# Performance work log

Measured on AMD Instinct MI355X. Metric: run time of the kernel, lower is better.

Reference implementation:

```python
import jax, jax.numpy as jnp
import numpy as np

SCALE = 0.02
EPS = 1e-5


def setup_inputs() -> dict:
    key = jax.random.key(0)
    ks = jax.random.split(key, 11)
    C = 256
    inp = {
        "x": jax.random.normal(ks[0], (64, C, 28, 28), dtype=jnp.float32),
        "w1": jax.random.normal(ks[1], (C, C, 3, 3), dtype=jnp.float32) * 0.05,
        "g1": jax.random.uniform(ks[2], (C,), dtype=jnp.float32, minval=0.5, maxval=1.5),
        "b1": jax.random.normal(ks[3], (C,), dtype=jnp.float32) * 0.1,
        "m1": jax.random.normal(ks[4], (C,), dtype=jnp.float32) * 0.1,
        "v1": jax.random.uniform(ks[5], (C,), dtype=jnp.float32, minval=0.5, maxval=1.5),
        "w2": jax.random.normal(ks[6], (C, C, 3, 3), dtype=jnp.float32) * 0.05,
        "g2": jax.random.uniform(ks[7], (C,), dtype=jnp.float32, minval=0.5, maxval=1.5),
        "b2": jax.random.normal(ks[8], (C,), dtype=jnp.float32) * 0.1,
        "m2": jax.random.normal(ks[9], (C,), dtype=jnp.float32) * 0.1,
        "v2": jax.random.uniform(ks[10], (C,), dtype=jnp.float32, minval=0.5, maxval=1.5),
    }
    return inp


def _bin_conv3x3(x, w, stride=1):
    # 1-bit weight conv: sign(w)*scale, straight-through estimator for grads.
    wb = w + jax.lax.stop_gradient(jnp.sign(w) - w)
    y = jax.lax.conv_general_dilated(
        x, wb,
        window_strides=(stride, stride),
        padding=[(1, 1), (1, 1)],
        dimension_numbers=("NCHW", "OIHW", "NCHW"),
    )
    return y * SCALE


def _bn(x, g, b, m, v):
    # eval-mode batchnorm with running stats
    inv = g * jax.lax.rsqrt(v + EPS)  # [C]
    return x * inv[None, :, None, None] + (b - m * inv)[None, :, None, None]


def reference(x, w1, g1, b1, m1, v1, w2, g2, b2, m2, v2):
    out = jax.nn.relu(_bn(_bin_conv3x3(x, w1, 1), g1, b1, m1, v1))
    out = _bn(_bin_conv3x3(out, w2, 1), g2, b2, m2, v2)
    return jax.nn.relu(out + x)
```

## Files before the change

### kernel.cpp

```cpp
#include <hip/hip_runtime.h>

#define EPS_F 1e-5f
#define SCALE_F 0.02f

using short8  = __attribute__((ext_vector_type(8))) short;
using floatx4 = __attribute__((ext_vector_type(4))) float;

__device__ __forceinline__ unsigned short f2bf(float f) {
  unsigned u = __float_as_uint(f);
  return (unsigned short)((u + 0x7fffu + ((u >> 16) & 1u)) >> 16);
}

__global__ void prep_w(const float* __restrict__ w1, const float* __restrict__ w2,
                       unsigned short* __restrict__ ap1, unsigned short* __restrict__ ap2,
                       const float* g1, const float* b1, const float* m1, const float* v1,
                       const float* g2, const float* b2, const float* m2, const float* v2,
                       float* bnp) {
  const float* __restrict__ w = blockIdx.y ? w2 : w1;
  unsigned short* __restrict__ ap = blockIdx.y ? ap2 : ap1;
  int t = blockIdx.x * 256 + threadIdx.x;
  int off = t >> 13;
  int c8  = (t >> 8) & 31;
  int co  = t & 255;
  const float* ws = w + (size_t)(co * 256 + c8 * 8) * 9 + off;
  short8 o;
#pragma unroll
  for (int j = 0; j < 8; ++j) {
    float v = ws[j * 9];
    o[j] = (v > 0.f) ? (short)0x3F80 : ((v < 0.f) ? (short)0xBF80 : (short)0);
  }
  *(short8*)(ap + (size_t)t * 8) = o;
  if (blockIdx.x == 0 && blockIdx.y == 0) {
    int c = threadIdx.x;
    float i1 = g1[c] * rsqrtf(v1[c] + EPS_F);
    bnp[c]       = SCALE_F * i1;
    bnp[256 + c] = b1[c] - m1[c] * i1;
    float i2 = g2[c] * rsqrtf(v2[c] + EPS_F);
    bnp[512 + c] = SCALE_F * i2;
    bnp[768 + c] = b2[c] - m2[c] * i2;
  }
}

__global__ void prep_x(const float* __restrict__ x, unsigned short* __restrict__ xb,
                       unsigned short* __restrict__ abuf) {
  int h = blockIdx.x;
  int n = blockIdx.y;
  int tid = threadIdx.x;
  const float* xs = x + ((size_t)n * 256 + tid) * 784 + h * 28;
  unsigned short* xd = xb + ((size_t)n * 900 + (h + 1) * 30 + 1) * 256 + tid;
#pragma unroll
  for (int p4 = 0; p4 < 7; ++p4) {
    floatx4 f = *(const floatx4*)(xs + p4 * 4);
#pragma unroll
    for (int k = 0; k < 4; ++k)
      xd[(size_t)(p4 * 4 + k) * 256] = f2bf(f[k]);
  }
  {
    int bufi = tid >> 7, side = (tid >> 6) & 1, c4 = tid & 63;
    unsigned short* bb = (bufi ? abuf : xb) + ((size_t)n * 900 + (h + 1) * 30 + side * 29) * 256;
    ushort4 z = {0, 0, 0, 0};
    *(ushort4*)(bb + c4 * 4) = z;
  }
  if (h == 0 || h == 27) {
    int row = (h == 0) ? 0 : 29;
    for (int u = tid; u < 3840; u += 256) {
      int bufi = u / 1920;
      int r    = u - bufi * 1920;
      int px   = r >> 6, c4 = r & 63;
      unsigned short* bb = (bufi ? abuf : xb) + ((size_t)n * 900 + row * 30 + px) * 256;
      ushort4 z = {0, 0, 0, 0};
      *(ushort4*)(bb + c4 * 4) = z;
    }
  }
}

template<int STAGE>
__global__ __launch_bounds__(256, 2) void bconv(
    const unsigned short* __restrict__ Bin,
    const unsigned short* __restrict__ Apack,
    const float* __restrict__ bnp,
    unsigned short* __restrict__ aout,
    const float* __restrict__ xres,
    float* __restrict__ out)
{
  __shared__ __align__(16) unsigned short smem[STAGE == 1 ? 29568 : 11520];
  unsigned short* Blds = smem;

  const int tid  = threadIdx.x;
  const int lane = tid & 63;
  const int wv   = tid >> 6;
  const int quad = lane >> 4;
  const int l16  = lane & 15;
  const int spBlk = blockIdx.x;
  const int n     = blockIdx.y;

  const int prow0 = 4 * spBlk;
  const unsigned short* bsrc = Bin + ((size_t)n * 900 + prow0 * 30) * 256;
  const int coW = wv * 64;

  int pxS[7];
#pragma unroll
  for (int s = 0; s < 7; ++s) {
    int lm = s * 16 + l16;
    int hl = lm / 28;
    int w  = lm - hl * 28;
    pxS[s] = hl * 30 + w;
  }

  floatx4 acc[4][7];
#pragma unroll
  for (int c = 0; c < 4; ++c)
#pragma unroll
    for (int s = 0; s < 7; ++s)
      acc[c][s] = (floatx4){0.f, 0.f, 0.f, 0.f};

#pragma unroll 1
  for (int cb = 0; cb < 4; ++cb) {
    __syncthreads();
    for (int u = tid; u < 1440; u += 256) {
      int px = u >> 3, c = u & 7;
      const unsigned short* src = bsrc + (size_t)px * 256 + cb * 64 + c * 8;
      *(short8*)&Blds[(px << 6) + ((c ^ (px & 7)) << 3)] = *(const short8*)src;
    }
    __syncthreads();

    const int cq = cb * 8 + quad;
#pragma unroll 1
    for (int kh = 0; kh < 3; ++kh) {
#pragma unroll
      for (int kw = 0; kw < 3; ++kw) {
        const int D = kh * 30 + kw;
        const int chunk0 = (kh * 3 + kw) * 32 + cq;
#pragma unroll
        for (int half = 0; half < 2; ++half) {
          const int chunk = chunk0 + half * 4;
          const unsigned short* apb = Apack + ((size_t)(chunk * 256 + coW + l16)) * 8;
          short8 a0 = *(const short8*)(apb);
          short8 a1 = *(const short8*)(apb + 16 * 8);
          short8 a2 = *(const short8*)(apb + 32 * 8);
          short8 a3 = *(const short8*)(apb + 48 * 8);
          const int C = half * 4 + quad;
#pragma unroll
          for (int s = 0; s < 7; ++s) {
            int pe = pxS[s] + D;
            short8 b = *(const short8*)&Blds[(pe << 6) + ((C ^ (pe & 7)) << 3)];
            acc[0][s] = __builtin_amdgcn_mfma_f32_16x16x32_bf16(a0, b, acc[0][s], 0, 0, 0);
            acc[1][s] = __builtin_amdgcn_mfma_f32_16x16x32_bf16(a1, b, acc[1][s], 0, 0, 0);
            acc[2][s] = __builtin_amdgcn_mfma_f32_16x16x32_bf16(a2, b, acc[2][s], 0, 0, 0);
            acc[3][s] = __builtin_amdgcn_mfma_f32_16x16x32_bf16(a3, b, acc[3][s], 0, 0, 0);
          }
        }
      }
    }
  }

  if (STAGE == 1) {
    __syncthreads();
#pragma unroll
    for (int c = 0; c < 4; ++c) {
      int co = coW + c * 16 + quad * 4;
      floatx4 As = *(const floatx4*)(bnp + co);
      floatx4 Bs = *(const floatx4*)(bnp + 256 + co);
#pragma unroll
      for (int s = 0; s < 7; ++s) {
        int px = s * 16 + l16;
        ushort4 o;
        o.x = f2bf(fmaxf(acc[c][s][0] * As[0] + Bs[0], 0.f));
        o.y = f2bf(fmaxf(acc[c][s][1] * As[1] + Bs[1], 0.f));
        o.z = f2bf(fmaxf(acc[c][s][2] * As[2] + Bs[2], 0.f));
        o.w = f2bf(fmaxf(acc[c][s][3] * As[3] + Bs[3], 0.f));
        *(ushort4*)&smem[px * 264 + co] = o;
      }
    }
    __syncthreads();
    unsigned short* dst0 = aout + ((size_t)n * 900 + (prow0 + 1) * 30 + 1) * 256;
    for (int u = tid; u < 3584; u += 256) {
      int px = u >> 5;
      int c8 = (u & 31) * 8;
      int r  = px / 28;
      int w  = px - r * 28;
      *(short8*)(dst0 + (size_t)(r * 30 + w) * 256 + c8) = *(const short8*)&smem[px * 264 + c8];
    }
  } else {
#pragma unroll
    for (int c = 0; c < 4; ++c) {
      int co = coW + c * 16 + quad * 4;
      floatx4 As = *(const floatx4*)(bnp + 512 + co);
      floatx4 Bs = *(const floatx4*)(bnp + 768 + co);
#pragma unroll
      for (int s = 0; s < 7; ++s) {
        int m = spBlk * 112 + s * 16 + l16;
#pragma unroll
        for (int r = 0; r < 4; ++r) {
          size_t oidx = ((size_t)n * 256 + co + r) * 784 + m;
          float v = acc[c][s][r] * As[r] + Bs[r] + xres[oidx];
          out[oidx] = fmaxf(v, 0.f);
        }
      }
    }
  }
}


extern "C" void kernel_launch(void* const* d_in, const int* in_sizes, int n_in,
                              void* d_out, int out_size, void* d_ws, size_t ws_size,
                              hipStream_t stream) {
  const float* x  = (const float*)d_in[0];
  const float* w1 = (const float*)d_in[1];
  const float* g1 = (const float*)d_in[2];
  const float* b1 = (const float*)d_in[3];
  const float* m1 = (const float*)d_in[4];
  const float* v1 = (const float*)d_in[5];
  const float* w2 = (const float*)d_in[6];
  const float* g2 = (const float*)d_in[7];
  const float* b2 = (const float*)d_in[8];
  const float* m2 = (const float*)d_in[9];
  const float* v2 = (const float*)d_in[10];
  float* out = (float*)d_out;

  char* ws = (char*)d_ws;
  const size_t PADBUF = (size_t)64 * 900 * 256 * 2;
  const size_t WPACK  = 589824ull * 2;
  unsigned short* xb   = (unsigned short*)ws;
  unsigned short* abuf = (unsigned short*)(ws + PADBUF);
  unsigned short* ap1  = (unsigned short*)(ws + 2 * PADBUF);
  unsigned short* ap2  = (unsigned short*)(ws + 2 * PADBUF + WPACK);
  float* bnp           = (float*)(ws + 2 * PADBUF + 2 * WPACK);

  prep_w<<<dim3(288, 2), 256, 0, stream>>>(w1, w2, ap1, ap2,
                                           g1, b1, m1, v1, g2, b2, m2, v2, bnp);
  prep_x<<<dim3(28, 64), 256, 0, stream>>>(x, xb, abuf);

  dim3 grid(7, 64);
  bconv<1><<<grid, 256, 0, stream>>>(xb,   ap1, bnp, abuf, nullptr, nullptr);
  bconv<2><<<grid, 256, 0, stream>>>(abuf, ap2, bnp, nullptr, x, out);
}
```

Before: 252.1 us.

## Retile conv blocks to two images by 128 channels and merge prep kernels

Each conv block now covers two images (224 pixels) and 128 output channels instead of one image and all 256 channels, and the grid gains a z dimension for the channel half. Each wave holds 2x14 accumulators instead of 4x7, so it loads half as many weight fragments per MFMA group and reuses each LDS B fragment across fewer MFMAs. The two prep kernels are fused into one launch to remove a launch. The trade-off is that more LDS B reads happen per MFMA, the activation tile is loaded twice (once per channel half), and stage 1 uses one smem size for both stages, which may affect occupancy.

```diff
diff --git a/kernel.cpp b/kernel.cpp
--- a/kernel.cpp
+++ b/kernel.cpp
@@ -11,41 +11,44 @@
   return (unsigned short)((u + 0x7fffu + ((u >> 16) & 1u)) >> 16);
 }
 
-__global__ void prep_w(const float* __restrict__ w1, const float* __restrict__ w2,
-                       unsigned short* __restrict__ ap1, unsigned short* __restrict__ ap2,
-                       const float* g1, const float* b1, const float* m1, const float* v1,
-                       const float* g2, const float* b2, const float* m2, const float* v2,
-                       float* bnp) {
-  const float* __restrict__ w = blockIdx.y ? w2 : w1;
-  unsigned short* __restrict__ ap = blockIdx.y ? ap2 : ap1;
-  int t = blockIdx.x * 256 + threadIdx.x;
-  int off = t >> 13;
-  int c8  = (t >> 8) & 31;
-  int co  = t & 255;
-  const float* ws = w + (size_t)(co * 256 + c8 * 8) * 9 + off;
-  short8 o;
-#pragma unroll
-  for (int j = 0; j < 8; ++j) {
-    float v = ws[j * 9];
-    o[j] = (v > 0.f) ? (short)0x3F80 : ((v < 0.f) ? (short)0xBF80 : (short)0);
-  }
-  *(short8*)(ap + (size_t)t * 8) = o;
-  if (blockIdx.x == 0 && blockIdx.y == 0) {
-    int c = threadIdx.x;
-    float i1 = g1[c] * rsqrtf(v1[c] + EPS_F);
-    bnp[c]       = SCALE_F * i1;
-    bnp[256 + c] = b1[c] - m1[c] * i1;
-    float i2 = g2[c] * rsqrtf(v2[c] + EPS_F);
-    bnp[512 + c] = SCALE_F * i2;
-    bnp[768 + c] = b2[c] - m2[c] * i2;
-  }
-}
-
-__global__ void prep_x(const float* __restrict__ x, unsigned short* __restrict__ xb,
-                       unsigned short* __restrict__ abuf) {
-  int h = blockIdx.x;
-  int n = blockIdx.y;
+__global__ void prep_all(const float* __restrict__ x,
+                         unsigned short* __restrict__ xb, unsigned short* __restrict__ abuf,
+                         const float* __restrict__ w1, const float* __restrict__ w2,
+                         unsigned short* __restrict__ ap1, unsigned short* __restrict__ ap2,
+                         const float* g1, const float* b1, const float* m1, const float* v1,
+                         const float* g2, const float* b2, const float* m2, const float* v2,
+                         float* bnp) {
+  int bid = blockIdx.x;
   int tid = threadIdx.x;
+  if (bid < 576) {
+    const float* __restrict__ w = (bid >= 288) ? w2 : w1;
+    unsigned short* __restrict__ ap = (bid >= 288) ? ap2 : ap1;
+    int t = (bid >= 288 ? bid - 288 : bid) * 256 + tid;
+    int off = t >> 13;
+    int c8  = (t >> 8) & 31;
+    int co  = t & 255;
+    const float* wsrc = w + (size_t)(co * 256 + c8 * 8) * 9 + off;
+    short8 o;
+#pragma unroll
+    for (int j = 0; j < 8; ++j) {
+      float v = wsrc[j * 9];
+      o[j] = (v > 0.f) ? (short)0x3F80 : ((v < 0.f) ? (short)0xBF80 : (short)0);
+    }
+    *(short8*)(ap + (size_t)t * 8) = o;
+    if (bid == 0) {
+      int c = tid;
+      float i1 = g1[c] * rsqrtf(v1[c] + EPS_F);
+      bnp[c]       = SCALE_F * i1;
+      bnp[256 + c] = b1[c] - m1[c] * i1;
+      float i2 = g2[c] * rsqrtf(v2[c] + EPS_F);
+      bnp[512 + c] = SCALE_F * i2;
+      bnp[768 + c] = b2[c] - m2[c] * i2;
+    }
+    return;
+  }
+  int bid2 = bid - 576;
+  int n = bid2 / 28;
+  int h = bid2 - n * 28;
   const float* xs = x + ((size_t)n * 256 + tid) * 784 + h * 28;
   unsigned short* xd = xb + ((size_t)n * 900 + (h + 1) * 30 + 1) * 256 + tid;
 #pragma unroll
@@ -83,7 +86,7 @@
     const float* __restrict__ xres,
     float* __restrict__ out)
 {
-  __shared__ __align__(16) unsigned short smem[STAGE == 1 ? 29568 : 11520];
+  __shared__ __align__(16) unsigned short smem[23040];
   unsigned short* Blds = smem;
 
   const int tid  = threadIdx.x;
@@ -92,34 +95,39 @@
   const int quad = lane >> 4;
   const int l16  = lane & 15;
   const int spBlk = blockIdx.x;
-  const int n     = blockIdx.y;
+  const int n0    = blockIdx.y * 2;
+  const int coB   = blockIdx.z;
+  const int coBase = coB * 128;
 
   const int prow0 = 4 * spBlk;
-  const unsigned short* bsrc = Bin + ((size_t)n * 900 + prow0 * 30) * 256;
-  const int coW = wv * 64;
-
-  int pxS[7];
-#pragma unroll
-  for (int s = 0; s < 7; ++s) {
-    int lm = s * 16 + l16;
-    int hl = lm / 28;
-    int w  = lm - hl * 28;
-    pxS[s] = hl * 30 + w;
-  }
-
-  floatx4 acc[4][7];
-#pragma unroll
-  for (int c = 0; c < 4; ++c)
-#pragma unroll
-    for (int s = 0; s < 7; ++s)
+  const unsigned short* bsrc = Bin + ((size_t)n0 * 900 + prow0 * 30) * 256;
+  const int coW = coBase + wv * 32;
+
+  int pxS[14];
+#pragma unroll
+  for (int s = 0; s < 14; ++s) {
+    int lm  = s * 16 + l16;
+    int img = lm >= 112;
+    int lmL = lm - 112 * img;
+    int hl  = lmL / 28;
+    int w   = lmL - hl * 28;
+    pxS[s] = img * 180 + hl * 30 + w;
+  }
+
+  floatx4 acc[2][14];
+#pragma unroll
+  for (int c = 0; c < 2; ++c)
+#pragma unroll
+    for (int s = 0; s < 14; ++s)
       acc[c][s] = (floatx4){0.f, 0.f, 0.f, 0.f};
 
 #pragma unroll 1
   for (int cb = 0; cb < 4; ++cb) {
     __syncthreads();
-    for (int u = tid; u < 1440; u += 256) {
+    for (int u = tid; u < 2880; u += 256) {
       int px = u >> 3, c = u & 7;
-      const unsigned short* src = bsrc + (size_t)px * 256 + cb * 64 + c * 8;
+      int imgo = (px >= 180) ? (230400 - 180 * 256) : 0;
+      const unsigned short* src = bsrc + imgo + (size_t)px * 256 + cb * 64 + c * 8;
       *(short8*)&Blds[(px << 6) + ((c ^ (px & 7)) << 3)] = *(const short8*)src;
     }
     __syncthreads();
@@ -137,17 +145,13 @@
           const unsigned short* apb = Apack + ((size_t)(chunk * 256 + coW + l16)) * 8;
           short8 a0 = *(const short8*)(apb);
           short8 a1 = *(const short8*)(apb + 16 * 8);
-          short8 a2 = *(const short8*)(apb + 32 * 8);
-          short8 a3 = *(const short8*)(apb + 48 * 8);
           const int C = half * 4 + quad;
 #pragma unroll
-          for (int s = 0; s < 7; ++s) {
+          for (int s = 0; s < 14; ++s) {
             int pe = pxS[s] + D;
             short8 b = *(const short8*)&Blds[(pe << 6) + ((C ^ (pe & 7)) << 3)];
             acc[0][s] = __builtin_amdgcn_mfma_f32_16x16x32_bf16(a0, b, acc[0][s], 0, 0, 0);
             acc[1][s] = __builtin_amdgcn_mfma_f32_16x16x32_bf16(a1, b, acc[1][s], 0, 0, 0);
-            acc[2][s] = __builtin_amdgcn_mfma_f32_16x16x32_bf16(a2, b, acc[2][s], 0, 0, 0);
-            acc[3][s] = __builtin_amdgcn_mfma_f32_16x16x32_bf16(a3, b, acc[3][s], 0, 0, 0);
           }
         }
       }
@@ -157,42 +161,51 @@
   if (STAGE == 1) {
     __syncthreads();
 #pragma unroll
-    for (int c = 0; c < 4; ++c) {
-      int co = coW + c * 16 + quad * 4;
-      floatx4 As = *(const floatx4*)(bnp + co);
-      floatx4 Bs = *(const floatx4*)(bnp + 256 + co);
-#pragma unroll
-      for (int s = 0; s < 7; ++s) {
-        int px = s * 16 + l16;
-        ushort4 o;
-        o.x = f2bf(fmaxf(acc[c][s][0] * As[0] + Bs[0], 0.f));
-        o.y = f2bf(fmaxf(acc[c][s][1] * As[1] + Bs[1], 0.f));
-        o.z = f2bf(fmaxf(acc[c][s][2] * As[2] + Bs[2], 0.f));
-        o.w = f2bf(fmaxf(acc[c][s][3] * As[3] + Bs[3], 0.f));
-        *(ushort4*)&smem[px * 264 + co] = o;
-      }
-    }
-    __syncthreads();
-    unsigned short* dst0 = aout + ((size_t)n * 900 + (prow0 + 1) * 30 + 1) * 256;
-    for (int u = tid; u < 3584; u += 256) {
-      int px = u >> 5;
-      int c8 = (u & 31) * 8;
-      int r  = px / 28;
-      int w  = px - r * 28;
-      *(short8*)(dst0 + (size_t)(r * 30 + w) * 256 + c8) = *(const short8*)&smem[px * 264 + c8];
+    for (int p = 0; p < 2; ++p) {
+#pragma unroll
+      for (int c = 0; c < 2; ++c) {
+        int co = coW + c * 16 + quad * 4;
+        floatx4 As = *(const floatx4*)(bnp + co);
+        floatx4 Bs = *(const floatx4*)(bnp + 256 + co);
+        int coL = co - coBase;
+#pragma unroll
+        for (int si = 0; si < 7; ++si) {
+          int s  = p * 7 + si;
+          int px = s * 16 + l16 - 112 * p;
+          ushort4 o;
+          o.x = f2bf(fmaxf(acc[c][s][0] * As[0] + Bs[0], 0.f));
+          o.y = f2bf(fmaxf(acc[c][s][1] * As[1] + Bs[1], 0.f));
+          o.z = f2bf(fmaxf(acc[c][s][2] * As[2] + Bs[2], 0.f));
+          o.w = f2bf(fmaxf(acc[c][s][3] * As[3] + Bs[3], 0.f));
+          *(ushort4*)&smem[px * 132 + coL] = o;
+        }
+      }
+      __syncthreads();
+      unsigned short* dst0 = aout + ((size_t)(n0 + p) * 900 + (prow0 + 1) * 30 + 1) * 256 + coBase;
+      for (int u = tid; u < 1792; u += 256) {
+        int px = u >> 4;
+        int c8 = (u & 15) * 8;
+        int r  = px / 28;
+        int w  = px - r * 28;
+        *(short8*)(dst0 + (size_t)(r * 30 + w) * 256 + c8) = *(const short8*)&smem[px * 132 + c8];
+      }
+      __syncthreads();
     }
   } else {
 #pragma unroll
-    for (int c = 0; c < 4; ++c) {
+    for (int c = 0; c < 2; ++c) {
       int co = coW + c * 16 + quad * 4;
       floatx4 As = *(const floatx4*)(bnp + 512 + co);
       floatx4 Bs = *(const floatx4*)(bnp + 768 + co);
 #pragma unroll
-      for (int s = 0; s < 7; ++s) {
-        int m = spBlk * 112 + s * 16 + l16;
+      for (int s = 0; s < 14; ++s) {
+        int lm  = s * 16 + l16;
+        int img = lm >= 112;
+        int lmL = lm - 112 * img;
+        int m   = spBlk * 112 + lmL;
 #pragma unroll
         for (int r = 0; r < 4; ++r) {
-          size_t oidx = ((size_t)n * 256 + co + r) * 784 + m;
+          size_t oidx = ((size_t)(n0 + img) * 256 + co + r) * 784 + m;
           float v = acc[c][s][r] * As[r] + Bs[r] + xres[oidx];
           out[oidx] = fmaxf(v, 0.f);
         }
@@ -227,11 +240,10 @@
   unsigned short* ap2  = (unsigned short*)(ws + 2 * PADBUF + WPACK);
   float* bnp           = (float*)(ws + 2 * PADBUF + 2 * WPACK);
 
-  prep_w<<<dim3(288, 2), 256, 0, stream>>>(w1, w2, ap1, ap2,
-                                           g1, b1, m1, v1, g2, b2, m2, v2, bnp);
-  prep_x<<<dim3(28, 64), 256, 0, stream>>>(x, xb, abuf);
-
-  dim3 grid(7, 64);
+  prep_all<<<2368, 256, 0, stream>>>(x, xb, abuf, w1, w2, ap1, ap2,
+                                     g1, b1, m1, v1, g2, b2, m2, v2, bnp);
+
+  dim3 grid(7, 32, 2);
   bconv<1><<<grid, 256, 0, stream>>>(xb,   ap1, bnp, abuf, nullptr, nullptr);
   bconv<2><<<grid, 256, 0, stream>>>(abuf, ap2, bnp, nullptr, x, out);
 }
```

Result: slower. 266.3 us (+5.6%).
